# Kernel optimization log

Measured on AMD Instinct MI355X. Metric: run time of the kernel, lower is better.

## Reference

```python
import jax, jax.numpy as jnp
import numpy as np

B, TE, TD, H = 8, 512, 256, 256  # batch, enc len, dec len, hidden (He==Hd)

def setup_inputs() -> dict:
    key = jax.random.key(0)
    k1, k2, k3, k4, k5 = jax.random.split(key, 5)
    # Keras 'uniform' initializer: U(-0.05, 0.05)
    u = lambda k, s: jax.random.uniform(k, s, jnp.float32, -0.05, 0.05)
    return {
        "encoder_out_seq": jax.random.normal(k1, (B, TE, H), jnp.float32),
        "decoder_out_seq": jax.random.normal(k2, (B, TD, H), jnp.float32),
        "W_a": u(k3, (H, H)),
        "U_a": u(k4, (H, H)),
        "V_a": u(k5, (H, 1)),
    }

def reference(encoder_out_seq, decoder_out_seq, W_a, U_a, V_a):
    # Bahdanau additive attention, fully batched (same math as the per-step K.rnn loop)
    We = jnp.einsum('bih,hk->bik', encoder_out_seq, W_a)   # [B,Te,H]
    Uh = jnp.einsum('bjh,hk->bjk', decoder_out_seq, U_a)   # [B,Td,H]
    # energies: V_a^T tanh(We_i + Uh_j)  -> [B,Td,Te]
    t = jnp.tanh(We[:, None, :, :] + Uh[:, :, None, :])    # [B,Td,Te,H]
    e = jnp.einsum('bjih,h->bji', t, V_a[:, 0])             # [B,Td,Te]
    e = jax.nn.softmax(e, axis=-1)                          # softmax over encoder positions
    c = jnp.einsum('bji,bih->bjh', e, encoder_out_seq)      # [B,Td,H]
    return (c, e)
```

## Files before the change

### kernel.cpp

```cpp
#include <hip/hip_runtime.h>


#define BB 8
#define TE 512
#define TD 256
#define HH 256

#define EXP2F(x) __builtin_amdgcn_exp2f(x)
#define RCPF(x)  __builtin_amdgcn_rcpf(x)
#define KSCALE   2.8853900817779268f
#define NSC      (-2.8853900817779268f)

__global__ __launch_bounds__(256) void k_pre(
    const float* __restrict__ enc, const float* __restrict__ dec,
    const float* __restrict__ Wa,  const float* __restrict__ Ua,
    float* __restrict__ W4, float* __restrict__ Uhe)
{
    const int tid = threadIdx.x;
    const bool is_enc = blockIdx.x < 256;
    const int bi = is_enc ? blockIdx.x : (blockIdx.x - 256);
    const int m0 = (bi >> 2) * 64;
    const int n0 = (bi & 3) * 64;
    const float* X = is_enc ? enc : dec;
    const float* W = is_enc ? Wa : Ua;

    __shared__ float Xs[32][68];
    __shared__ float Ws[32][68];

    const int kq = tid & 7,  xr = tid >> 3;
    const int wk = tid >> 3, wn = (tid & 7) * 8;
    const int tx = tid & 15, ty = tid >> 4;

    float acc[4][4];
    #pragma unroll
    for (int r = 0; r < 4; r++)
        #pragma unroll
        for (int c = 0; c < 4; c++) acc[r][c] = 0.f;

    for (int kc = 0; kc < HH; kc += 32) {
        float4 xa = *(const float4*)(X + (size_t)(m0 + xr) * HH + kc + kq * 4);
        float4 xb = *(const float4*)(X + (size_t)(m0 + xr + 32) * HH + kc + kq * 4);
        float4 wa = *(const float4*)(W + (size_t)(kc + wk) * HH + n0 + wn);
        float4 wb = *(const float4*)(W + (size_t)(kc + wk) * HH + n0 + wn + 4);
        __syncthreads();
        Xs[kq * 4 + 0][xr] = xa.x; Xs[kq * 4 + 1][xr] = xa.y;
        Xs[kq * 4 + 2][xr] = xa.z; Xs[kq * 4 + 3][xr] = xa.w;
        Xs[kq * 4 + 0][xr + 32] = xb.x; Xs[kq * 4 + 1][xr + 32] = xb.y;
        Xs[kq * 4 + 2][xr + 32] = xb.z; Xs[kq * 4 + 3][xr + 32] = xb.w;
        *(float4*)&Ws[wk][wn]     = wa;
        *(float4*)&Ws[wk][wn + 4] = wb;
        __syncthreads();
        #pragma unroll
        for (int k = 0; k < 32; k++) {
            float4 a = *(const float4*)&Xs[k][ty * 4];
            float4 b = *(const float4*)&Ws[k][tx * 4];
            acc[0][0] = fmaf(a.x, b.x, acc[0][0]); acc[0][1] = fmaf(a.x, b.y, acc[0][1]);
            acc[0][2] = fmaf(a.x, b.z, acc[0][2]); acc[0][3] = fmaf(a.x, b.w, acc[0][3]);
            acc[1][0] = fmaf(a.y, b.x, acc[1][0]); acc[1][1] = fmaf(a.y, b.y, acc[1][1]);
            acc[1][2] = fmaf(a.y, b.z, acc[1][2]); acc[1][3] = fmaf(a.y, b.w, acc[1][3]);
            acc[2][0] = fmaf(a.z, b.x, acc[2][0]); acc[2][1] = fmaf(a.z, b.y, acc[2][1]);
            acc[2][2] = fmaf(a.z, b.z, acc[2][2]); acc[2][3] = fmaf(a.z, b.w, acc[2][3]);
            acc[3][0] = fmaf(a.w, b.x, acc[3][0]); acc[3][1] = fmaf(a.w, b.y, acc[3][1]);
            acc[3][2] = fmaf(a.w, b.z, acc[3][2]); acc[3][3] = fmaf(a.w, b.w, acc[3][3]);
        }
    }

    if (is_enc) {
        const int b  = m0 >> 9;
        const int ib = (m0 & 511) + ty * 4;
        const int hq = (n0 >> 2) + tx;
        float* dst = W4 + (((size_t)b * 64 + hq) * TE + ib) * 4;
        #pragma unroll
        for (int r = 0; r < 4; r++) {
            float4 v;
            v.x = EXP2F(acc[r][0] * KSCALE); v.y = EXP2F(acc[r][1] * KSCALE);
            v.z = EXP2F(acc[r][2] * KSCALE); v.w = EXP2F(acc[r][3] * KSCALE);
            *(float4*)(dst + (size_t)r * 4) = v;
        }
    } else {
        #pragma unroll
        for (int r = 0; r < 4; r++) {
            float4 v;
            v.x = EXP2F(acc[r][0] * KSCALE); v.y = EXP2F(acc[r][1] * KSCALE);
            v.z = EXP2F(acc[r][2] * KSCALE); v.w = EXP2F(acc[r][3] * KSCALE);
            *(float4*)(Uhe + (size_t)(m0 + ty * 4 + r) * HH + n0 + tx * 4) = v;
        }
    }
}

__global__ __launch_bounds__(512) void k_attn(
    const float* __restrict__ enc, const float* __restrict__ W4,
    const float* __restrict__ Uhe, const float* __restrict__ Va,
    float* __restrict__ out_c, float* __restrict__ out_e)
{
    const int wv = threadIdx.x >> 6, lane = threadIdx.x & 63;
    const int b   = blockIdx.x & 7;
    const int j0  = (blockIdx.x >> 3) * 4;
    const int jj0 = b * TD + j0;

    __shared__ float sP[4][TE];
    __shared__ float sR[8][4][HH];

    const int i = (wv << 6) + lane;
    const float* wp = W4 + ((size_t)b * 64 * TE + i) * 4;
    const float* ua = Uhe + (size_t)jj0 * HH;
    const float* va = Va;

    float a0 = 0.f, a1 = 0.f, a2 = 0.f, a3 = 0.f;

#define QSTEP(ACC, U)                                                     \
    {                                                                     \
        float A_ = fmaf(w4.x, (U).x, 1.f);                                \
        float B_ = fmaf(w4.y, (U).y, 1.f);                                \
        float C_ = fmaf(w4.z, (U).z, 1.f);                                \
        float D_ = fmaf(w4.w, (U).w, 1.f);                                \
        float dAB = A_ * B_, dCD = C_ * D_;                               \
        float nAB = fmaf(v4.x, B_, v4.y * A_);                            \
        float nCD = fmaf(v4.z, D_, v4.w * C_);                            \
        float num = fmaf(nAB, dCD, nCD * dAB);                            \
        ACC = fmaf(num, RCPF(dAB * dCD), ACC);                            \
    }

    #pragma unroll 2
    for (int q = 0; q < 64; q++) {
        float4 w4 = *(const float4*)(wp + (size_t)q * TE * 4);
        float4 v4 = *(const float4*)(va + 4 * q);
        float4 u0 = *(const float4*)(ua + 4 * q);
        float4 u1 = *(const float4*)(ua + HH + 4 * q);
        float4 u2 = *(const float4*)(ua + 2 * HH + 4 * q);
        float4 u3 = *(const float4*)(ua + 3 * HH + 4 * q);
        QSTEP(a0, u0)
        QSTEP(a1, u1)
        QSTEP(a2, u2)
        QSTEP(a3, u3)
    }
#undef QSTEP

    sP[0][i] = NSC * a0;
    sP[1][i] = NSC * a1;
    sP[2][i] = NSC * a2;
    sP[3][i] = NSC * a3;
    __syncthreads();

    if (wv < 4) {
        float ev[8];
        float m = -3.0e38f;
        #pragma unroll
        for (int k = 0; k < 8; k++) {
            ev[k] = sP[wv][lane + 64 * k];
            m = fmaxf(m, ev[k]);
        }
        #pragma unroll
        for (int off = 32; off; off >>= 1) m = fmaxf(m, __shfl_xor(m, off, 64));
        float s = 0.f;
        #pragma unroll
        for (int k = 0; k < 8; k++) { ev[k] = EXP2F(ev[k] - m); s += ev[k]; }
        #pragma unroll
        for (int off = 32; off; off >>= 1) s += __shfl_xor(s, off, 64);
        float rs = RCPF(s);
        float* oe = out_e + (size_t)(jj0 + wv) * TE;
        #pragma unroll
        for (int k = 0; k < 8; k++) {
            float p = ev[k] * rs;
            sP[wv][lane + 64 * k] = p;
            oe[lane + 64 * k] = p;
        }
    }
    __syncthreads();

    const int ib = wv << 6;
    const float* eb = enc + ((size_t)b * TE + ib) * HH + 4 * lane;
    float4 c0 = {0,0,0,0}, c1 = {0,0,0,0}, c2 = {0,0,0,0}, c3 = {0,0,0,0};
    #pragma unroll 2
    for (int k = 0; k < 64; k++) {
        float p0 = sP[0][ib + k];
        float p1 = sP[1][ib + k];
        float p2 = sP[2][ib + k];
        float p3 = sP[3][ib + k];
        float4 q = *(const float4*)(eb + (size_t)k * HH);
        c0.x = fmaf(p0, q.x, c0.x); c0.y = fmaf(p0, q.y, c0.y);
        c0.z = fmaf(p0, q.z, c0.z); c0.w = fmaf(p0, q.w, c0.w);
        c1.x = fmaf(p1, q.x, c1.x); c1.y = fmaf(p1, q.y, c1.y);
        c1.z = fmaf(p1, q.z, c1.z); c1.w = fmaf(p1, q.w, c1.w);
        c2.x = fmaf(p2, q.x, c2.x); c2.y = fmaf(p2, q.y, c2.y);
        c2.z = fmaf(p2, q.z, c2.z); c2.w = fmaf(p2, q.w, c2.w);
        c3.x = fmaf(p3, q.x, c3.x); c3.y = fmaf(p3, q.y, c3.y);
        c3.z = fmaf(p3, q.z, c3.z); c3.w = fmaf(p3, q.w, c3.w);
    }
    *(float4*)&sR[wv][0][4 * lane] = c0;
    *(float4*)&sR[wv][1][4 * lane] = c1;
    *(float4*)&sR[wv][2][4 * lane] = c2;
    *(float4*)&sR[wv][3][4 * lane] = c3;
    __syncthreads();

    {
        const int jr = wv & 3;
        const int h2 = (wv >> 2) * 128 + 2 * lane;
        float sx = 0.f, sy = 0.f;
        #pragma unroll
        for (int ww = 0; ww < 8; ww++) {
            float2 t = *(const float2*)&sR[ww][jr][h2];
            sx += t.x; sy += t.y;
        }
        float2 o; o.x = sx; o.y = sy;
        *(float2*)(out_c + (size_t)(jj0 + jr) * HH + h2) = o;
    }
}

extern "C" void kernel_launch(void* const* d_in, const int* in_sizes, int n_in,
                              void* d_out, int out_size, void* d_ws, size_t ws_size,
                              hipStream_t stream) {
    const float* enc = (const float*)d_in[0];
    const float* dec = (const float*)d_in[1];
    const float* Wa  = (const float*)d_in[2];
    const float* Ua  = (const float*)d_in[3];
    const float* Va  = (const float*)d_in[4];

    float* W4  = (float*)d_ws;
    float* Uhe = W4 + (size_t)BB * HH * TE;

    float* out_c = (float*)d_out;
    float* out_e = out_c + (size_t)BB * TD * HH;

    k_pre<<<384, 256, 0, stream>>>(enc, dec, Wa, Ua, W4, Uhe);
    k_attn<<<BB * TD / 4, 512, 0, stream>>>(enc, W4, Uhe, Va, out_c, out_e);
}
```

Before: 113.6 us.

## Store exp(We) and encoder in fp16 and merge eight terms per reciprocal

The precompute kernel now writes exp2(We) as fp16 in an 8-wide interleaved layout and adds extra blocks that convert the encoder to fp16. The attention kernel loads these half-precision operands, which halves their memory traffic. It also combines eight tanh-rational terms per reciprocal instead of four, cutting the number of rcp instructions. The cost is fp16 rounding and a wider range for the product of eight denominators, which could overflow or lose accuracy.

Result: no change. 114.9 us (+1.1%).

```diff
diff --git a/kernel.cpp b/kernel.cpp
--- a/kernel.cpp
+++ b/kernel.cpp
@@ -11,12 +11,30 @@
 #define KSCALE   2.8853900817779268f
 #define NSC      (-2.8853900817779268f)
 
+typedef _Float16 h4 __attribute__((ext_vector_type(4)));
+typedef _Float16 h8 __attribute__((ext_vector_type(8)));
+
 __global__ __launch_bounds__(256) void k_pre(
     const float* __restrict__ enc, const float* __restrict__ dec,
     const float* __restrict__ Wa,  const float* __restrict__ Ua,
-    float* __restrict__ W4, float* __restrict__ Uhe)
+    _Float16* __restrict__ W4h, float* __restrict__ Uhe,
+    _Float16* __restrict__ enc16)
 {
     const int tid = threadIdx.x;
+
+    if (blockIdx.x >= 384) {
+        const size_t base = (size_t)(blockIdx.x - 384) * 16384;
+        #pragma unroll 4
+        for (int t = 0; t < 16; t++) {
+            size_t idx = base + ((size_t)t * 256 + tid) * 4;
+            float4 v = *(const float4*)(enc + idx);
+            h4 o; o.x = (_Float16)v.x; o.y = (_Float16)v.y;
+            o.z = (_Float16)v.z; o.w = (_Float16)v.w;
+            *(h4*)(enc16 + idx) = o;
+        }
+        return;
+    }
+
     const bool is_enc = blockIdx.x < 256;
     const int bi = is_enc ? blockIdx.x : (blockIdx.x - 256);
     const int m0 = (bi >> 2) * 64;
@@ -68,14 +86,17 @@
     if (is_enc) {
         const int b  = m0 >> 9;
         const int ib = (m0 & 511) + ty * 4;
-        const int hq = (n0 >> 2) + tx;
-        float* dst = W4 + (((size_t)b * 64 + hq) * TE + ib) * 4;
+        const int hh = n0 + tx * 4;
+        const int o  = hh >> 3;
+        const int hf = (hh & 7);
         #pragma unroll
         for (int r = 0; r < 4; r++) {
-            float4 v;
-            v.x = EXP2F(acc[r][0] * KSCALE); v.y = EXP2F(acc[r][1] * KSCALE);
-            v.z = EXP2F(acc[r][2] * KSCALE); v.w = EXP2F(acc[r][3] * KSCALE);
-            *(float4*)(dst + (size_t)r * 4) = v;
+            h4 v;
+            v.x = (_Float16)EXP2F(acc[r][0] * KSCALE);
+            v.y = (_Float16)EXP2F(acc[r][1] * KSCALE);
+            v.z = (_Float16)EXP2F(acc[r][2] * KSCALE);
+            v.w = (_Float16)EXP2F(acc[r][3] * KSCALE);
+            *(h4*)(W4h + (((size_t)b * 32 + o) * TE + ib + r) * 8 + hf) = v;
         }
     } else {
         #pragma unroll
@@ -89,7 +110,7 @@
 }
 
 __global__ __launch_bounds__(512) void k_attn(
-    const float* __restrict__ enc, const float* __restrict__ W4,
+    const _Float16* __restrict__ enc16, const _Float16* __restrict__ W4h,
     const float* __restrict__ Uhe, const float* __restrict__ Va,
     float* __restrict__ out_c, float* __restrict__ out_e)
 {
@@ -102,39 +123,58 @@
     __shared__ float sR[8][4][HH];
 
     const int i = (wv << 6) + lane;
-    const float* wp = W4 + ((size_t)b * 64 * TE + i) * 4;
+    const _Float16* wp = W4h + ((size_t)b * 32 * TE + i) * 8;
     const float* ua = Uhe + (size_t)jj0 * HH;
     const float* va = Va;
 
     float a0 = 0.f, a1 = 0.f, a2 = 0.f, a3 = 0.f;
 
-#define QSTEP(ACC, U)                                                     \
+#define OSTEP(ACC, UA, UB)                                                \
     {                                                                     \
-        float A_ = fmaf(w4.x, (U).x, 1.f);                                \
-        float B_ = fmaf(w4.y, (U).y, 1.f);                                \
-        float C_ = fmaf(w4.z, (U).z, 1.f);                                \
-        float D_ = fmaf(w4.w, (U).w, 1.f);                                \
-        float dAB = A_ * B_, dCD = C_ * D_;                               \
-        float nAB = fmaf(v4.x, B_, v4.y * A_);                            \
-        float nCD = fmaf(v4.z, D_, v4.w * C_);                            \
-        float num = fmaf(nAB, dCD, nCD * dAB);                            \
-        ACC = fmaf(num, RCPF(dAB * dCD), ACC);                            \
+        float A0 = fmaf(w0, (UA).x, 1.f);                                 \
+        float A1 = fmaf(w1, (UA).y, 1.f);                                 \
+        float A2 = fmaf(w2, (UA).z, 1.f);                                 \
+        float A3 = fmaf(w3, (UA).w, 1.f);                                 \
+        float A4 = fmaf(w4, (UB).x, 1.f);                                 \
+        float A5 = fmaf(w5, (UB).y, 1.f);                                 \
+        float A6 = fmaf(w6, (UB).z, 1.f);                                 \
+        float A7 = fmaf(w7, (UB).w, 1.f);                                 \
+        float dab = A0 * A1, dcd = A2 * A3;                               \
+        float def_ = A4 * A5, dgh = A6 * A7;                              \
+        float nab = fmaf(v4a.x, A1, v4a.y * A0);                          \
+        float ncd = fmaf(v4a.z, A3, v4a.w * A2);                          \
+        float nef = fmaf(v4b.x, A5, v4b.y * A4);                          \
+        float ngh = fmaf(v4b.z, A7, v4b.w * A6);                          \
+        float den4a = dab * dcd,  den4b = def_ * dgh;                     \
+        float num4a = fmaf(nab, dcd, ncd * dab);                          \
+        float num4b = fmaf(nef, dgh, ngh * def_);                         \
+        float num = fmaf(num4a, den4b, num4b * den4a);                    \
+        ACC = fmaf(num, RCPF(den4a * den4b), ACC);                        \
     }
 
     #pragma unroll 2
-    for (int q = 0; q < 64; q++) {
-        float4 w4 = *(const float4*)(wp + (size_t)q * TE * 4);
-        float4 v4 = *(const float4*)(va + 4 * q);
-        float4 u0 = *(const float4*)(ua + 4 * q);
-        float4 u1 = *(const float4*)(ua + HH + 4 * q);
-        float4 u2 = *(const float4*)(ua + 2 * HH + 4 * q);
-        float4 u3 = *(const float4*)(ua + 3 * HH + 4 * q);
-        QSTEP(a0, u0)
-        QSTEP(a1, u1)
-        QSTEP(a2, u2)
-        QSTEP(a3, u3)
-    }
-#undef QSTEP
+    for (int q = 0; q < 32; q++) {
+        h8 w8 = *(const h8*)(wp + (size_t)q * TE * 8);
+        float w0 = (float)w8[0], w1 = (float)w8[1];
+        float w2 = (float)w8[2], w3 = (float)w8[3];
+        float w4 = (float)w8[4], w5 = (float)w8[5];
+        float w6 = (float)w8[6], w7 = (float)w8[7];
+        float4 v4a = *(const float4*)(va + 8 * q);
+        float4 v4b = *(const float4*)(va + 8 * q + 4);
+        float4 u0a = *(const float4*)(ua + 8 * q);
+        float4 u0b = *(const float4*)(ua + 8 * q + 4);
+        float4 u1a = *(const float4*)(ua + HH + 8 * q);
+        float4 u1b = *(const float4*)(ua + HH + 8 * q + 4);
+        float4 u2a = *(const float4*)(ua + 2 * HH + 8 * q);
+        float4 u2b = *(const float4*)(ua + 2 * HH + 8 * q + 4);
+        float4 u3a = *(const float4*)(ua + 3 * HH + 8 * q);
+        float4 u3b = *(const float4*)(ua + 3 * HH + 8 * q + 4);
+        OSTEP(a0, u0a, u0b)
+        OSTEP(a1, u1a, u1b)
+        OSTEP(a2, u2a, u2b)
+        OSTEP(a3, u3a, u3b)
+    }
+#undef OSTEP
 
     sP[0][i] = NSC * a0;
     sP[1][i] = NSC * a1;
@@ -169,7 +209,7 @@
     __syncthreads();
 
     const int ib = wv << 6;
-    const float* eb = enc + ((size_t)b * TE + ib) * HH + 4 * lane;
+    const _Float16* eb = enc16 + ((size_t)b * TE + ib) * HH + 4 * lane;
     float4 c0 = {0,0,0,0}, c1 = {0,0,0,0}, c2 = {0,0,0,0}, c3 = {0,0,0,0};
     #pragma unroll 2
     for (int k = 0; k < 64; k++) {
@@ -177,15 +217,17 @@
         float p1 = sP[1][ib + k];
         float p2 = sP[2][ib + k];
         float p3 = sP[3][ib + k];
-        float4 q = *(const float4*)(eb + (size_t)k * HH);
-        c0.x = fmaf(p0, q.x, c0.x); c0.y = fmaf(p0, q.y, c0.y);
-        c0.z = fmaf(p0, q.z, c0.z); c0.w = fmaf(p0, q.w, c0.w);
-        c1.x = fmaf(p1, q.x, c1.x); c1.y = fmaf(p1, q.y, c1.y);
-        c1.z = fmaf(p1, q.z, c1.z); c1.w = fmaf(p1, q.w, c1.w);
-        c2.x = fmaf(p2, q.x, c2.x); c2.y = fmaf(p2, q.y, c2.y);
-        c2.z = fmaf(p2, q.z, c2.z); c2.w = fmaf(p2, q.w, c2.w);
-        c3.x = fmaf(p3, q.x, c3.x); c3.y = fmaf(p3, q.y, c3.y);
-        c3.z = fmaf(p3, q.z, c3.z); c3.w = fmaf(p3, q.w, c3.w);
+        h4 q16 = *(const h4*)(eb + (size_t)k * HH);
+        float qx = (float)q16.x, qy = (float)q16.y;
+        float qz = (float)q16.z, qw = (float)q16.w;
+        c0.x = fmaf(p0, qx, c0.x); c0.y = fmaf(p0, qy, c0.y);
+        c0.z = fmaf(p0, qz, c0.z); c0.w = fmaf(p0, qw, c0.w);
+        c1.x = fmaf(p1, qx, c1.x); c1.y = fmaf(p1, qy, c1.y);
+        c1.z = fmaf(p1, qz, c1.z); c1.w = fmaf(p1, qw, c1.w);
+        c2.x = fmaf(p2, qx, c2.x); c2.y = fmaf(p2, qy, c2.y);
+        c2.z = fmaf(p2, qz, c2.z); c2.w = fmaf(p2, qw, c2.w);
+        c3.x = fmaf(p3, qx, c3.x); c3.y = fmaf(p3, qy, c3.y);
+        c3.z = fmaf(p3, qz, c3.z); c3.w = fmaf(p3, qw, c3.w);
     }
     *(float4*)&sR[wv][0][4 * lane] = c0;
     *(float4*)&sR[wv][1][4 * lane] = c1;
@@ -216,12 +258,13 @@
     const float* Ua  = (const float*)d_in[3];
     const float* Va  = (const float*)d_in[4];
 
-    float* W4  = (float*)d_ws;
-    float* Uhe = W4 + (size_t)BB * HH * TE;
+    _Float16* W4h   = (_Float16*)d_ws;
+    _Float16* enc16 = W4h + (size_t)BB * HH * TE;
+    float*    Uhe   = (float*)(enc16 + (size_t)BB * TE * HH);
 
     float* out_c = (float*)d_out;
     float* out_e = out_c + (size_t)BB * TD * HH;
 
-    k_pre<<<384, 256, 0, stream>>>(enc, dec, Wa, Ua, W4, Uhe);
-    k_attn<<<BB * TD / 4, 512, 0, stream>>>(enc, W4, Uhe, Va, out_c, out_e);
+    k_pre<<<448, 256, 0, stream>>>(enc, dec, Wa, Ua, W4h, Uhe, enc16);
+    k_attn<<<BB * TD / 4, 512, 0, stream>>>(enc16, W4h, Uhe, Va, out_c, out_e);
 }
```
